# Optimization experiments

Measured on AMD Instinct MI355X. Metric: run time of the kernel, lower is better.

The kernel has to match this reference:

```python
import jax, jax.numpy as jnp
import numpy as np

B, N, P_CTR, K = 16, 2048, 256, 32
H, W = 24, 80
INFEA = 64
MLP = [64, 128, 128, 256]
DIST = 0.5
EPS = 1e-5


def setup_inputs() -> dict:
    key = jax.random.key(0)
    ks = jax.random.split(key, 12)
    inp = {}
    inp['pc'] = jax.random.normal(ks[0], (B, 3, N), jnp.float32)
    inp['feat'] = jax.random.normal(ks[1], (B, INFEA, N), jnp.float32)
    inp['img1'] = jax.random.normal(ks[2], (B, MLP[0], H, W), jnp.float32)
    inp['img2'] = jax.random.normal(ks[3], (B, MLP[1], H, W), jnp.float32)
    inp['P'] = jax.random.normal(ks[4], (B, 3, 4), jnp.float32)
    inp['query_v1'] = jax.random.randint(ks[5], (B, N), 0, H * W, dtype=jnp.int32)
    inp['new_pc'] = jax.random.normal(ks[6], (B, 3, P_CTR), jnp.float32)
    dims = [INFEA + 3] + MLP  # conv chain: 67->64->128->128->256, 1x1 convs, no bias
    for i in range(4):
        fan_in = dims[i]
        inp[f'w{i+1}'] = jax.random.normal(ks[7 + i], (dims[i + 1], dims[i]), jnp.float32) * np.sqrt(2.0 / fan_in)
        inp[f'g{i+1}'] = jnp.ones((dims[i + 1],), jnp.float32)   # BN gamma, init 1
        inp[f'b{i+1}'] = jnp.zeros((dims[i + 1],), jnp.float32)  # BN beta, init 0
    return inp


def query_depth_point(pc, new_pc, dist, k):
    # depth (z-axis) ball query: pc (B,3,N), new_pc (B,3,P) -> idx (B,P,k) int32, num (B,P)
    dz = jnp.abs(pc[:, 2, None, :] - new_pc[:, 2, :, None])  # (B,P,N)
    mask = dz < dist
    num = jnp.sum(mask, axis=-1).astype(jnp.int32)           # neighbor count per center
    # stable argsort of ~mask puts valid indices first, in ascending original order
    order = jnp.argsort(jnp.logical_not(mask), axis=-1, stable=True)
    idx = order[..., :k]
    slot_valid = jnp.arange(k)[None, None, :] < jnp.minimum(num, k)[..., None]
    idx = jnp.where(slot_valid, idx, idx[..., :1])           # pad with first valid index
    return idx.astype(jnp.int32), num


def gather_ch(x, idx):
    # x (B,C,M), idx (B,L) -> (B,C,L)
    return jnp.take_along_axis(x, idx[:, None, :], axis=2)


def conv_bn_relu(x, w, g, b):
    # 1x1 conv (no bias) + BatchNorm2d (training-mode batch stats) + ReLU
    y = jnp.einsum('oc,bcnk->bonk', w, x)
    m = jnp.mean(y, axis=(0, 2, 3), keepdims=True)
    v = jnp.var(y, axis=(0, 2, 3), keepdims=True)
    y = (y - m) * jax.lax.rsqrt(v + EPS)
    y = y * g[None, :, None, None] + b[None, :, None, None]
    return jax.nn.relu(y)


def reference(pc, feat, img1, img2, P, query_v1, new_pc,
              w1, g1, b1, w2, g2, b2, w3, g3, b3, w4, g4, b4):
    idx, num = query_depth_point(pc, new_pc, DIST, K)       # (B,P,K), (B,P)
    idx_flat = idx.reshape(B, P_CTR * K)
    idx_rgb = jnp.take_along_axis(query_v1, idx_flat, axis=1)  # (B,P*K) pixel ids

    grouped_pc = gather_ch(pc, idx_flat).reshape(B, 3, P_CTR, K) - new_pc[:, :, :, None]
    grouped_feat = gather_ch(feat, idx_flat).reshape(B, INFEA, P_CTR, K)
    rgb1 = gather_ch(img1.reshape(B, MLP[0], H * W), idx_rgb).reshape(B, MLP[0], P_CTR, K)
    rgb2 = gather_ch(img2.reshape(B, MLP[1], H * W), idx_rgb).reshape(B, MLP[1], P_CTR, K)

    grouped = jnp.concatenate([grouped_pc, grouped_feat], axis=1)  # (B,67,P,K)
    pf = conv_bn_relu(grouped, w1, g1, b1)                         # (B,64,P,K)
    f1 = jnp.concatenate([pf, rgb1], axis=1)                       # (B,128,P,K)
    pf = conv_bn_relu(pf, w2, g2, b2)                              # (B,128,P,K)
    f2 = jnp.concatenate([pf, rgb2], axis=1)                       # (B,256,P,K)
    pf = conv_bn_relu(pf, w3, g3, b3)
    pf = conv_bn_relu(pf, w4, g4, b4)                              # (B,256,P,K)
    out = jnp.concatenate([f1, f2, pf], axis=1)                    # (B,640,P,K)
    valid = (num > 0).reshape(B, 1, P_CTR, 1).astype(out.dtype)
    return out * valid
```

## Files before the change

### kernel.cpp

```cpp
#include <hip/hip_runtime.h>
#include <hip/hip_fp16.h>

#define BB 16
#define NN 2048
#define PC 256
#define KK 32
#define HWS 1920
#define PT (BB*PC*KK)
#define EPSF 1e-5f
#define THR 512

#define CH_IDXR 256
#define CH_IDX  257
#define CH_VAL  258
#define CH_FT   356
#define STATS_OFF ((size_t)259 << 13)

typedef _Float16 f16x8 __attribute__((ext_vector_type(8)));
typedef float    f32x4 __attribute__((ext_vector_type(4)));

__device__ __forceinline__ unsigned packh2(float lo, float hi) {
  unsigned a = (unsigned)__half_as_ushort(__float2half(lo));
  unsigned b = (unsigned)__half_as_ushort(__float2half(hi));
  return a | (b << 16);
}
__device__ __forceinline__ float h2lo(unsigned u) {
  return __half2float(__ushort_as_half((unsigned short)(u & 0xffffu)));
}
__device__ __forceinline__ float h2hi(unsigned u) {
  return __half2float(__ushort_as_half((unsigned short)(u >> 16)));
}
__device__ __forceinline__ void nt_store4(float* p, float4 v) {
  __builtin_nontemporal_store(v.x, p);
  __builtin_nontemporal_store(v.y, p+1);
  __builtin_nontemporal_store(v.z, p+2);
  __builtin_nontemporal_store(v.w, p+3);
}
__device__ __forceinline__ void nt_store1(float* p, float v) {
  __builtin_nontemporal_store(v, p);
}

__global__ __launch_bounds__(256,2) void k_prep(
    const float* __restrict__ feat, float* out)
{
  __shared__ float tile[64][261];
  int tid = threadIdx.x;
  int b = blockIdx.x >> 3, n0 = (blockIdx.x & 7) << 8;
  #pragma unroll 8
  for (int c = 0; c < 64; c++)
    tile[c][tid] = feat[((size_t)b*64 + c)*NN + n0 + tid];
  __syncthreads();
  unsigned* ftw = (unsigned*)out + (((size_t)b*640 + CH_FT)<<13);
  #pragma unroll
  for (int e = tid; e < 256*32; e += 256) {
    int q = e & 31, nl = e >> 5;
    ftw[(size_t)(n0 + nl)*32 + q] = packh2(tile[2*q][nl], tile[2*q+1][nl]);
  }
}

template<bool WSC>
__global__ __launch_bounds__(256) void k_idx(
    const float* __restrict__ pc, const float* __restrict__ npc,
    const int* __restrict__ qv1, float* out, int* __restrict__ wsi)
{
  __shared__ int slots[4][KK];
  int tid = threadIdx.x;
  if (blockIdx.x < 5) {
    int i = blockIdx.x*256 + tid;
    if (i < 1152) out[STATS_OFF + i] = 0.0f;
  }
  int wl = tid >> 6, lane = tid & 63;
  int w = blockIdx.x*4 + wl;
  int b = w >> 8, p = w & 255;
  if (lane == 0) slots[wl][0] = 0;
  float zc = npc[(b*3+2)*PC + p];
  const float* pz = pc + ((size_t)b*3+2)*NN;
  int num = 0;
  for (int ci=0; ci<NN/64; ci++) {
    int n = ci*64 + lane;
    bool m = fabsf(pz[n] - zc) < 0.5f;
    unsigned long long mk = __ballot(m);
    if (m) {
      int rank = num + __popcll(mk & ((1ull<<lane)-1ull));
      if (rank < KK) slots[wl][rank] = n;
    }
    num += __popcll(mk);
  }
  __syncthreads();
  if (lane < KK) {
    int nj = (lane < num) ? slots[wl][lane] : slots[wl][0];
    size_t col = (size_t)p*KK + lane;
    int enc = (num > 0) ? qv1[b*NN + nj] : -1;
    ((int*)out)[(((size_t)b*640 + CH_IDX )<<13) + col] = nj;
    ((int*)out)[(((size_t)b*640 + CH_IDXR)<<13) + col] = enc;
    if constexpr (WSC) wsi[(size_t)b*8192 + col] = enc;
  }
  if (lane == 0)
    out[(((size_t)b*640 + CH_VAL)<<13) + (size_t)p*KK] = (num > 0) ? 1.0f : 0.0f;
}

template<int CIN, int CINP, int COUT, int BOCH, int WVP, int WVO, int WFP, int WFO,
         int XMODE, int XBASE, int YMODE, int YBASE, int STIN, int STOUT,
         int SWZ, int QR, int PFB, int TILES>
__global__ __launch_bounds__(THR,4) void k_mfma(
    const float* __restrict__ pc, const float* __restrict__ npc,
    const float* __restrict__ W,
    const float* __restrict__ g, const float* __restrict__ bv,
    const float* __restrict__ go, const float* __restrict__ bo,
    float* out)
{
  constexpr int KC = CINP/32;
  constexpr int KCIN = (XMODE == 1) ? CIN/32 : 1;
  __shared__ __align__(16) _Float16 xs[2][128*QR*2];
  __shared__ float scs[128], shs[128];
  __shared__ float redu[WVP*BOCH*2];
  __shared__ float ost[(YMODE==3) ? 2*BOCH : 1];

  int tid = threadIdx.x;
  int tile0 = blockIdx.x * TILES;
  int b = tile0 >> 6;
  int och0 = blockIdx.y * BOCH;

  int wv = tid >> 6, lane = tid & 63;
  int wp = wv % WVP, wo = wv / WVP;
  int lr = lane & 15, lg = lane >> 4;
  int prow0 = wp*(WFP*16), orow0 = wo*(WFO*16);

  unsigned rg[(XMODE==0)?8:1];
  float    pa = 0.f, pb = 0.f, na = 0.f, nb = 0.f;
  uint4    rgv[KCIN];

  auto LOADR = [&](int t) {
    int col0t = ((tile0 + t) & 63) << 7;
    if constexpr (XMODE == 0) {
      int posl = tid & 127, qb0 = tid >> 7;
      int n = ((const int*)out)[(((size_t)b*640 + CH_IDX)<<13) + col0t + posl];
      const unsigned* ftw = (const unsigned*)out + (((size_t)b*640 + CH_FT)<<13);
      #pragma unroll
      for (int k = 0; k < 8; k++)
        rg[k] = ftw[(size_t)n*32 + qb0 + 4*k];
      int pcol = (col0t + posl) >> 5;
      pa = pb = na = nb = 0.f;
      if (qb0 == 0) {
        pa = pc[((size_t)b*3+0)*NN + n]; na = npc[(b*3+0)*PC + pcol];
        pb = pc[((size_t)b*3+1)*NN + n]; nb = npc[(b*3+1)*PC + pcol];
      } else if (qb0 == 1) {
        pa = pc[((size_t)b*3+2)*NN + n]; na = npc[(b*3+2)*PC + pcol];
      }
    } else {
      #pragma unroll
      for (int k = 0; k < KCIN; k++) {
        int e = tid + k*THR;
        int q = e >> 5, pg = e & 31;
        rgv[k] = *(const uint4*)&((const unsigned*)out)[(((size_t)b*640 + XBASE + q)<<13) + col0t + pg*4];
      }
    }
  };

  auto STORE = [&](int t) {
    int col0t = ((tile0 + t) & 63) << 7;
    unsigned* xw = (unsigned*)xs[t & 1];
    if constexpr (XMODE == 0) {
      int posl = tid & 127, qb0 = tid >> 7;
      #pragma unroll
      for (int k = 0; k < 8; k++) {
        int q = qb0 + 4*k;
        int qs = (((q>>2) ^ ((posl>>2) & SWZ)) << 2) | (q & 3);
        xw[posl*QR + qs] = rg[k];
      }
      #pragma unroll
      for (int k = 8; k < 12; k++) {
        int q = qb0 + 4*k;
        unsigned u = 0u;
        if (k == 8) {
          if (qb0 == 0)      u = packh2(pa - na, pb - nb);
          else if (qb0 == 1) u = packh2(pa - na, 0.f);
        }
        int qs = (((q>>2) ^ ((posl>>2) & SWZ)) << 2) | (q & 3);
        xw[posl*QR + qs] = u;
      }
    } else {
      #pragma unroll
      for (int k = 0; k < KCIN; k++) {
        int e = tid + k*THR;
        int q = e >> 5, pg = e & 31;
        uint4 u = rgv[k];
        float s0 = scs[2*q], h0 = shs[2*q], s1 = scs[2*q+1], h1 = shs[2*q+1];
        unsigned uu[4] = {u.x, u.y, u.z, u.w};
        float lo_a[4], hi_a[4];
        #pragma unroll
        for (int j = 0; j < 4; j++) {
          lo_a[j] = fmaxf(fmaf(h2lo(uu[j]), s0, h0), 0.f);
          hi_a[j] = fmaxf(fmaf(h2hi(uu[j]), s1, h1), 0.f);
          int p = pg*4 + j;
          xw[p*QR + ((((q>>2) ^ ((p>>2) & SWZ)) << 2) | (q & 3))] = packh2(lo_a[j], hi_a[j]);
        }
        if constexpr (PFB >= 0) {
          float vv = out[(((size_t)b*640 + CH_VAL)<<13) + col0t + ((pg >> 3) << 5)];
          float4 L  = {lo_a[0]*vv, lo_a[1]*vv, lo_a[2]*vv, lo_a[3]*vv};
          float4 Hh = {hi_a[0]*vv, hi_a[1]*vv, hi_a[2]*vv, hi_a[3]*vv};
          size_t pb2 = (((size_t)b*640 + PFB + 2*q)<<13) + col0t + pg*4;
          nt_store4(&out[pb2],           L);
          nt_store4(&out[pb2 + (1<<13)], Hh);
        }
      }
    }
  };

  LOADR(0);

  f16x8 bfr[KC][WFO];
  #pragma unroll
  for (int kc = 0; kc < KC; kc++)
    #pragma unroll
    for (int fo = 0; fo < WFO; fo++) {
      int orow = och0 + orow0 + fo*16 + lr;
      f16x8 tf;
      if constexpr (XMODE == 0) {
        #pragma unroll
        for (int j = 0; j < 8; j++) {
          int c = kc*32 + lg*8 + j;
          int r = (c < 64) ? c + 3 : (c < 67 ? c - 64 : -1);
          tf[j] = (_Float16)((r >= 0) ? W[(size_t)orow*CIN + r] : 0.f);
        }
      } else {
        const float* wr = W + (size_t)orow*CIN + kc*32 + lg*8;
        float4 w0 = *(const float4*)wr;
        float4 w1 = *(const float4*)(wr + 4);
        tf[0]=(_Float16)w0.x; tf[1]=(_Float16)w0.y; tf[2]=(_Float16)w0.z; tf[3]=(_Float16)w0.w;
        tf[4]=(_Float16)w1.x; tf[5]=(_Float16)w1.y; tf[6]=(_Float16)w1.z; tf[7]=(_Float16)w1.w;
      }
      bfr[kc][fo] = tf;
    }

  if constexpr (XMODE == 1) {
    const float* stin = out + STATS_OFF + STIN;
    for (int c = tid; c < CIN; c += THR) {
      float m   = stin[c] * (1.0f/PT);
      float var = stin[CIN+c]*(1.0f/PT) - m*m;
      float s = rsqrtf(var + EPSF) * g[c];
      scs[c] = s; shs[c] = bv[c] - m*s;
    }
  }
  if constexpr (YMODE == 3) {
    const float* sto = out + STATS_OFF + STOUT;
    for (int i = tid; i < 2*BOCH; i += THR) {
      int gi = (i < BOCH) ? (och0 + i) : (COUT + och0 + (i - BOCH));
      ost[i] = sto[gi];
    }
  }
  __syncthreads();
  float osc_[WFO], osh_[WFO];
  if constexpr (YMODE == 3) {
    #pragma unroll
    for (int fo = 0; fo < WFO; fo++) {
      int oloc = orow0 + fo*16 + lr;
      float m   = ost[oloc]*(1.0f/PT);
      float var = ost[BOCH+oloc]*(1.0f/PT) - m*m;
      float s = rsqrtf(var + EPSF) * go[och0 + oloc];
      osc_[fo] = s; osh_[fo] = bo[och0 + oloc] - m*s;
    }
  }

  STORE(0);
  __syncthreads();

  float ssum[WFO], ssq[WFO];
  #pragma unroll
  for (int fo = 0; fo < WFO; fo++) { ssum[fo] = 0.f; ssq[fo] = 0.f; }

  #pragma unroll
  for (int t = 0; t < TILES; t++) {
    int col0t = ((tile0 + t) & 63) << 7;
    const _Float16* xb = xs[t & 1];

    if (t + 1 < TILES) LOADR(t + 1);

    f32x4 acc[WFP][WFO];
    const f32x4 zero4 = {0.f, 0.f, 0.f, 0.f};
    #pragma unroll
    for (int fp = 0; fp < WFP; fp++)
      #pragma unroll
      for (int fo = 0; fo < WFO; fo++) acc[fp][fo] = zero4;

    #pragma unroll
    for (int kc = 0; kc < KC; kc++) {
      f16x8 af[WFP];
      #pragma unroll
      for (int fp = 0; fp < WFP; fp++) {
        int row = prow0 + fp*16 + lr;
        int qb = (kc*4 + lg) ^ ((row>>2) & SWZ);
        af[fp] = *(const f16x8*)&xb[row*(QR*2) + qb*8];
      }
      #pragma unroll
      for (int fp = 0; fp < WFP; fp++)
        #pragma unroll
        for (int fo = 0; fo < WFO; fo++)
          acc[fp][fo] = __builtin_amdgcn_mfma_f32_16x16x32_f16(af[fp], bfr[kc][fo], acc[fp][fo], 0, 0, 0);
    }

    if constexpr (YMODE == 1) {
      #pragma unroll
      for (int fp = 0; fp < WFP; fp++) {
        int pos = col0t + prow0 + fp*16 + lg*4;
        #pragma unroll
        for (int fo = 0; fo < WFO; fo++) {
          float pr0 = __shfl_xor(acc[fp][fo][0], 1);
          float pr1 = __shfl_xor(acc[fp][fo][1], 1);
          float pr2 = __shfl_xor(acc[fp][fo][2], 1);
          float pr3 = __shfl_xor(acc[fp][fo][3], 1);
          if (!(lane & 1)) {
            uint4 u;
            u.x = packh2(acc[fp][fo][0], pr0); u.y = packh2(acc[fp][fo][1], pr1);
            u.z = packh2(acc[fp][fo][2], pr2); u.w = packh2(acc[fp][fo][3], pr3);
            int qrow = (och0 + orow0 + fo*16 + lr) >> 1;
            *(uint4*)&((unsigned*)out)[(((size_t)b*640 + YBASE + qrow)<<13) + pos] = u;
          }
        }
      }
    } else if constexpr (YMODE == 3) {
      #pragma unroll
      for (int fp = 0; fp < WFP; fp++) {
        int pos = col0t + prow0 + fp*16 + lg*4;
        float v = out[(((size_t)b*640 + CH_VAL)<<13) + (pos & ~31)];
        #pragma unroll
        for (int fo = 0; fo < WFO; fo++) {
          int och = och0 + orow0 + fo*16 + lr;
          float4 wvv;
          wvv.x = fmaxf(fmaf(acc[fp][fo][0], osc_[fo], osh_[fo]), 0.f) * v;
          wvv.y = fmaxf(fmaf(acc[fp][fo][1], osc_[fo], osh_[fo]), 0.f) * v;
          wvv.z = fmaxf(fmaf(acc[fp][fo][2], osc_[fo], osh_[fo]), 0.f) * v;
          wvv.w = fmaxf(fmaf(acc[fp][fo][3], osc_[fo], osh_[fo]), 0.f) * v;
          nt_store4(&out[(((size_t)b*640 + YBASE + och)<<13) + pos], wvv);
        }
      }
    }

    if constexpr (YMODE != 3) {
      #pragma unroll
      for (int fo = 0; fo < WFO; fo++)
        #pragma unroll
        for (int fp = 0; fp < WFP; fp++)
          #pragma unroll
          for (int r = 0; r < 4; r++) {
            float v = acc[fp][fo][r];
            ssum[fo] += v; ssq[fo] += v*v;
          }
    }

    if (t + 1 < TILES) STORE(t + 1);
    __syncthreads();
  }

  if constexpr (YMODE != 3) {
    #pragma unroll
    for (int fo = 0; fo < WFO; fo++) {
      float s = ssum[fo], q2 = ssq[fo];
      s  += __shfl_down(s, 32);  s  += __shfl_down(s, 16);
      q2 += __shfl_down(q2, 32); q2 += __shfl_down(q2, 16);
      if (lane < 16) {
        int oloc = orow0 + fo*16 + lane;
        redu[(wp*BOCH + oloc)*2]     = s;
        redu[(wp*BOCH + oloc)*2 + 1] = q2;
      }
    }
    __syncthreads();
    float* stg = out + STATS_OFF + STOUT;
    for (int i = tid; i < BOCH; i += THR) {
      float ss = 0.f, qq = 0.f;
      #pragma unroll
      for (int p = 0; p < WVP; p++) { ss += redu[(p*BOCH + i)*2]; qq += redu[(p*BOCH + i)*2 + 1]; }
      atomicAdd(&stg[och0 + i], ss);
      atomicAdd(&stg[COUT + och0 + i], qq);
    }
  }
}

__global__ __launch_bounds__(512) void k_rgb_lds(
    const float* __restrict__ img1, const float* __restrict__ img2,
    const int* __restrict__ wsi, float* out)
{
  __shared__ float ls[4][HWS];
  int tid = threadIdx.x;
  int b = blockIdx.x / 48, gq = blockIdx.x % 48;
  int gc0 = gq * 4;
  for (int e = tid; e < 4*(HWS/4); e += 512) {
    int c = e / (HWS/4), off = e % (HWS/4);
    int gc = gc0 + c;
    const float* src = (gc < 64) ? img1 + ((size_t)b*64 + gc)*HWS
                                 : img2 + ((size_t)b*128 + (gc-64))*HWS;
    *(float4*)&ls[c][off*4] = *(const float4*)&src[off*4];
  }
  __syncthreads();
  const int* idr = wsi + (size_t)b*8192;
  int dch0 = (gc0 < 64) ? 64 + gc0 : 256 + (gc0 - 64);
  for (int pp = tid; pp < 8192; pp += 512) {
    int enc = idr[pp];
    float v = (enc >= 0) ? 1.0f : 0.0f;
    int ir  = (enc >= 0) ? enc : 0;
    #pragma unroll
    for (int c = 0; c < 4; c++)
      nt_store1(&out[(((size_t)b*640 + dch0 + c)<<13) + pp], ls[c][ir] * v);
  }
}

__global__ __launch_bounds__(256) void k_rgb_fb(
    const float* __restrict__ img1, const float* __restrict__ img2, float* out)
{
  int tid = threadIdx.x;
  int pos = blockIdx.x*256 + tid;
  int b = pos >> 13, rem = pos & 8191;
  int enc = ((const int*)out)[(((size_t)b*640 + CH_IDXR)<<13) + rem];
  float v  = (enc >= 0) ? 1.0f : 0.0f;
  int  ir  = (enc >= 0) ? enc : 0;
  size_t o1 = (((size_t)b*640 + 64)<<13) + rem;
  const float* i1 = img1 + (size_t)b*64*HWS + ir;
  #pragma unroll 8
  for (int c=0;c<64;c++) out[o1 + ((size_t)c<<13)] = i1[(size_t)c*HWS] * v;
  size_t o2 = (((size_t)b*640 + 256)<<13) + rem;
  const float* i2 = img2 + (size_t)b*128*HWS + ir;
  #pragma unroll 8
  for (int c=0;c<128;c++) out[o2 + ((size_t)c<<13)] = i2[(size_t)c*HWS] * v;
}

extern "C" void kernel_launch(void* const* d_in, const int* in_sizes, int n_in,
                              void* d_out, int out_size, void* d_ws, size_t ws_size,
                              hipStream_t stream)
{
  const float* pc   = (const float*)d_in[0];
  const float* feat = (const float*)d_in[1];
  const float* img1 = (const float*)d_in[2];
  const float* img2 = (const float*)d_in[3];
  const int*   qv1  = (const int*)d_in[5];
  const float* npc  = (const float*)d_in[6];
  const float* w1 = (const float*)d_in[7];
  const float* g1 = (const float*)d_in[8];
  const float* b1 = (const float*)d_in[9];
  const float* w2 = (const float*)d_in[10];
  const float* g2 = (const float*)d_in[11];
  const float* b2 = (const float*)d_in[12];
  const float* w3 = (const float*)d_in[13];
  const float* g3 = (const float*)d_in[14];
  const float* b3 = (const float*)d_in[15];
  const float* w4 = (const float*)d_in[16];
  const float* g4 = (const float*)d_in[17];
  const float* b4 = (const float*)d_in[18];
  float* out = (float*)d_out;
  int*  wsi = (int*)d_ws;
  const bool use_ws = (d_ws != nullptr) && (ws_size >= (size_t)BB*8192*4);

  k_prep <<<128,256,0,stream>>>(feat, out);
  if (use_ws) k_idx<true ><<<1024,256,0,stream>>>(pc, npc, qv1, out, wsi);
  else        k_idx<false><<<1024,256,0,stream>>>(pc, npc, qv1, out, wsi);
  k_mfma<67,96,64,64,    2,4,4,1, 0,0,   1,324, 0,0,     0,48, -1,1>
      <<<dim3(1024,1),THR,0,stream>>>(pc,npc,w1,g1,b1,g1,b1,out);
  k_mfma<64,64,128,128,  2,4,4,2, 1,324, 1,260, 0,128,   7,36, 0,1>
      <<<dim3(1024,1),THR,0,stream>>>(pc,npc,w2,g1,b1,g1,b1,out);
  k_mfma<128,128,128,128,2,4,4,2, 1,260, 1,64,  128,384, 7,68, 128,1>
      <<<dim3(1024,1),THR,0,stream>>>(pc,npc,w3,g2,b2,g2,b2,out);
  k_mfma<128,128,256,128,2,4,4,2, 1,64,  2,0,   384,640, 7,68, -1,1>
      <<<dim3(1024,2),THR,0,stream>>>(pc,npc,w4,g3,b3,g3,b3,out);
  k_mfma<128,128,256,128,2,4,4,2, 1,64,  3,384, 384,640, 7,68, -1,1>
      <<<dim3(1024,2),THR,0,stream>>>(pc,npc,w4,g3,b3,g4,b4,out);
  if (use_ws) k_rgb_lds<<<768,512,0,stream>>>(img1, img2, wsi, out);
  else        k_rgb_fb <<<512,256,0,stream>>>(img1, img2, out);
}
```

Measured before the change: 579.1 us.

## Move intermediates to workspace, fuse RGB gather into conv3, two tiles per block

Intermediate fp16 activations, validity flags and BN stats now live in a separate workspace instead of scratch channels inside the output tensor. The RGB image gather is merged into the conv3 launch by interleaving extra gather blocks (3 of every 5) with conv blocks, so it runs alongside the GEMM work and one launch disappears. Every conv kernel now processes two tiles per block at half the grid size. The cost is a larger workspace requirement, a fallback path kept for small workspaces, and more complex block-role dispatch with shared memory overlaid between the two roles.

```diff
diff --git a/kernel.cpp b/kernel.cpp
--- a/kernel.cpp
+++ b/kernel.cpp
@@ -61,16 +61,19 @@
 template<bool WSC>
 __global__ __launch_bounds__(256) void k_idx(
     const float* __restrict__ pc, const float* __restrict__ npc,
-    const int* __restrict__ qv1, float* out, int* __restrict__ wsi)
+    const int* __restrict__ qv1, float* out, int* __restrict__ wsi,
+    float* __restrict__ wsval, float* __restrict__ wsst)
 {
   __shared__ int slots[4][KK];
   int tid = threadIdx.x;
-  if (blockIdx.x < 5) {
-    int i = blockIdx.x*256 + tid;
+  int bx = blockIdx.x;
+  if (bx < 5) {
+    int i = bx*256 + tid;
     if (i < 1152) out[STATS_OFF + i] = 0.0f;
+    if (wsst && i < 1152) wsst[i] = 0.0f;
   }
   int wl = tid >> 6, lane = tid & 63;
-  int w = blockIdx.x*4 + wl;
+  int w = bx*4 + wl;
   int b = w >> 8, p = w & 255;
   if (lane == 0) slots[wl][0] = 0;
   float zc = npc[(b*3+2)*PC + p];
@@ -95,29 +98,79 @@
     ((int*)out)[(((size_t)b*640 + CH_IDXR)<<13) + col] = enc;
     if constexpr (WSC) wsi[(size_t)b*8192 + col] = enc;
   }
-  if (lane == 0)
-    out[(((size_t)b*640 + CH_VAL)<<13) + (size_t)p*KK] = (num > 0) ? 1.0f : 0.0f;
-}
-
-template<int CIN, int CINP, int COUT, int BOCH, int WVP, int WVO, int WFP, int WFO,
-         int XMODE, int XBASE, int YMODE, int YBASE, int STIN, int STOUT,
-         int SWZ, int QR, int PFB, int TILES>
+  if (lane == 0) {
+    float v = (num > 0) ? 1.0f : 0.0f;
+    out[(((size_t)b*640 + CH_VAL)<<13) + (size_t)p*KK] = v;
+    if constexpr (WSC) if (wsval) wsval[(size_t)b*8192 + (size_t)p*KK] = v;
+  }
+}
+
+template<int CIN,int CINP,int COUT,int BOCH,int WVP,int WVO,int WFP,int WFO,
+         int XMODE,int YMODE,int SWZ,int QR,bool HASPF,int TILES,
+         int XROWS,int YROWS,int VROWS,int RGBN>
 __global__ __launch_bounds__(THR,4) void k_mfma(
     const float* __restrict__ pc, const float* __restrict__ npc,
     const float* __restrict__ W,
     const float* __restrict__ g, const float* __restrict__ bv,
     const float* __restrict__ go, const float* __restrict__ bo,
-    float* out)
+    const float* __restrict__ stin_p, float* __restrict__ stout_p,
+    const unsigned* __restrict__ xbuf, unsigned* __restrict__ ybuf,
+    float* __restrict__ yf32, float* __restrict__ pfb,
+    const float* __restrict__ valb,
+    const float* __restrict__ img1, const float* __restrict__ img2,
+    const int* __restrict__ wsi, float* out)
 {
   constexpr int KC = CINP/32;
   constexpr int KCIN = (XMODE == 1) ? CIN/32 : 1;
-  __shared__ __align__(16) _Float16 xs[2][128*QR*2];
-  __shared__ float scs[128], shs[128];
-  __shared__ float redu[WVP*BOCH*2];
-  __shared__ float ost[(YMODE==3) ? 2*BOCH : 1];
+  constexpr size_t XS_B = (size_t)128*QR*8;
+  constexpr size_t SC_B = 1024;
+  constexpr size_t RD_B = (size_t)WVP*BOCH*2*4;
+  constexpr size_t OS_B = (YMODE==3) ? (size_t)2*BOCH*4 : 16;
+  constexpr size_t CONV_B = XS_B + SC_B + RD_B + OS_B;
+  constexpr size_t RGB_B  = (RGBN>0) ? (size_t)4*HWS*4 : 0;
+  constexpr size_t SM_B   = (CONV_B > RGB_B) ? CONV_B : RGB_B;
+  __shared__ __align__(16) char smraw[SM_B];
 
   int tid = threadIdx.x;
-  int tile0 = blockIdx.x * TILES;
+  int bx = blockIdx.x;
+  int cid;
+  if constexpr (RGBN > 0) {
+    int m5 = bx % 5;
+    if (m5 >= 2) {
+      int rid = (bx/5)*3 + (m5-2);
+      float (*ls)[HWS] = (float(*)[HWS])smraw;
+      int b2 = rid / 48, gq = rid % 48;
+      int gc0 = gq*4;
+      for (int e = tid; e < 4*(HWS/4); e += THR) {
+        int c = e/(HWS/4), off = e%(HWS/4);
+        int gc = gc0 + c;
+        const float* src = (gc < 64) ? img1 + ((size_t)b2*64 + gc)*HWS
+                                     : img2 + ((size_t)b2*128 + (gc-64))*HWS;
+        *(float4*)&ls[c][off*4] = *(const float4*)&src[off*4];
+      }
+      __syncthreads();
+      const int* idr = wsi + (size_t)b2*8192;
+      int dch0 = (gc0 < 64) ? 64 + gc0 : 256 + (gc0 - 64);
+      for (int pp = tid; pp < 8192; pp += THR) {
+        int enc = idr[pp];
+        float v = (enc >= 0) ? 1.0f : 0.0f;
+        int ir  = (enc >= 0) ? enc : 0;
+        #pragma unroll
+        for (int c = 0; c < 4; c++)
+          nt_store1(&out[(((size_t)b2*640 + dch0 + c)<<13) + pp], ls[c][ir] * v);
+      }
+      return;
+    }
+    cid = (bx/5)*2 + m5;
+  } else cid = bx;
+
+  _Float16* xsb = (_Float16*)smraw;
+  float* scs  = (float*)(smraw + XS_B);
+  float* shs  = scs + 128;
+  float* redu = (float*)(smraw + XS_B + SC_B);
+  float* ost  = (float*)(smraw + XS_B + SC_B + RD_B);
+
+  int tile0 = cid * TILES;
   int b = tile0 >> 6;
   int och0 = blockIdx.y * BOCH;
 
@@ -152,14 +205,14 @@
       for (int k = 0; k < KCIN; k++) {
         int e = tid + k*THR;
         int q = e >> 5, pg = e & 31;
-        rgv[k] = *(const uint4*)&((const unsigned*)out)[(((size_t)b*640 + XBASE + q)<<13) + col0t + pg*4];
+        rgv[k] = *(const uint4*)&xbuf[(((size_t)b*XROWS + q)<<13) + col0t + pg*4];
       }
     }
   };
 
   auto STORE = [&](int t) {
     int col0t = ((tile0 + t) & 63) << 7;
-    unsigned* xw = (unsigned*)xs[t & 1];
+    unsigned* xw = (unsigned*)(xsb + (t & 1)*(128*QR*2));
     if constexpr (XMODE == 0) {
       int posl = tid & 127, qb0 = tid >> 7;
       #pragma unroll
@@ -195,13 +248,13 @@
           int p = pg*4 + j;
           xw[p*QR + ((((q>>2) ^ ((p>>2) & SWZ)) << 2) | (q & 3))] = packh2(lo_a[j], hi_a[j]);
         }
-        if constexpr (PFB >= 0) {
-          float vv = out[(((size_t)b*640 + CH_VAL)<<13) + col0t + ((pg >> 3) << 5)];
+        if constexpr (HASPF) {
+          float vv = valb[(((size_t)b*VROWS)<<13) + col0t + ((pg >> 3) << 5)];
           float4 L  = {lo_a[0]*vv, lo_a[1]*vv, lo_a[2]*vv, lo_a[3]*vv};
           float4 Hh = {hi_a[0]*vv, hi_a[1]*vv, hi_a[2]*vv, hi_a[3]*vv};
-          size_t pb2 = (((size_t)b*640 + PFB + 2*q)<<13) + col0t + pg*4;
-          nt_store4(&out[pb2],           L);
-          nt_store4(&out[pb2 + (1<<13)], Hh);
+          size_t pb2 = (((size_t)b*640 + 2*q)<<13) + col0t + pg*4;
+          nt_store4(&pfb[pb2],           L);
+          nt_store4(&pfb[pb2 + (1<<13)], Hh);
         }
       }
     }
@@ -234,19 +287,17 @@
     }
 
   if constexpr (XMODE == 1) {
-    const float* stin = out + STATS_OFF + STIN;
     for (int c = tid; c < CIN; c += THR) {
-      float m   = stin[c] * (1.0f/PT);
-      float var = stin[CIN+c]*(1.0f/PT) - m*m;
+      float m   = stin_p[c] * (1.0f/PT);
+      float var = stin_p[CIN+c]*(1.0f/PT) - m*m;
       float s = rsqrtf(var + EPSF) * g[c];
       scs[c] = s; shs[c] = bv[c] - m*s;
     }
   }
   if constexpr (YMODE == 3) {
-    const float* sto = out + STATS_OFF + STOUT;
     for (int i = tid; i < 2*BOCH; i += THR) {
       int gi = (i < BOCH) ? (och0 + i) : (COUT + och0 + (i - BOCH));
-      ost[i] = sto[gi];
+      ost[i] = stout_p[gi];
     }
   }
   __syncthreads();
@@ -272,7 +323,7 @@
   #pragma unroll
   for (int t = 0; t < TILES; t++) {
     int col0t = ((tile0 + t) & 63) << 7;
-    const _Float16* xb = xs[t & 1];
+    const _Float16* xb = xsb + (t & 1)*(128*QR*2);
 
     if (t + 1 < TILES) LOADR(t + 1);
 
@@ -314,7 +365,7 @@
             u.x = packh2(acc[fp][fo][0], pr0); u.y = packh2(acc[fp][fo][1], pr1);
             u.z = packh2(acc[fp][fo][2], pr2); u.w = packh2(acc[fp][fo][3], pr3);
             int qrow = (och0 + orow0 + fo*16 + lr) >> 1;
-            *(uint4*)&((unsigned*)out)[(((size_t)b*640 + YBASE + qrow)<<13) + pos] = u;
+            *(uint4*)&ybuf[(((size_t)b*YROWS + qrow)<<13) + pos] = u;
           }
         }
       }
@@ -322,7 +373,7 @@
       #pragma unroll
       for (int fp = 0; fp < WFP; fp++) {
         int pos = col0t + prow0 + fp*16 + lg*4;
-        float v = out[(((size_t)b*640 + CH_VAL)<<13) + (pos & ~31)];
+        float v = valb[(((size_t)b*VROWS)<<13) + (pos & ~31)];
         #pragma unroll
         for (int fo = 0; fo < WFO; fo++) {
           int och = och0 + orow0 + fo*16 + lr;
@@ -331,7 +382,7 @@
           wvv.y = fmaxf(fmaf(acc[fp][fo][1], osc_[fo], osh_[fo]), 0.f) * v;
           wvv.z = fmaxf(fmaf(acc[fp][fo][2], osc_[fo], osh_[fo]), 0.f) * v;
           wvv.w = fmaxf(fmaf(acc[fp][fo][3], osc_[fo], osh_[fo]), 0.f) * v;
-          nt_store4(&out[(((size_t)b*640 + YBASE + och)<<13) + pos], wvv);
+          nt_store4(&yf32[(((size_t)b*640 + och)<<13) + pos], wvv);
         }
       }
     }
@@ -365,13 +416,12 @@
       }
     }
     __syncthreads();
-    float* stg = out + STATS_OFF + STOUT;
     for (int i = tid; i < BOCH; i += THR) {
       float ss = 0.f, qq = 0.f;
       #pragma unroll
       for (int p = 0; p < WVP; p++) { ss += redu[(p*BOCH + i)*2]; qq += redu[(p*BOCH + i)*2 + 1]; }
-      atomicAdd(&stg[och0 + i], ss);
-      atomicAdd(&stg[COUT + och0 + i], qq);
+      atomicAdd(&stout_p[och0 + i], ss);
+      atomicAdd(&stout_p[COUT + och0 + i], qq);
     }
   }
 }
@@ -427,6 +477,7 @@
                               void* d_out, int out_size, void* d_ws, size_t ws_size,
                               hipStream_t stream)
 {
+  (void)in_sizes; (void)n_in;
   const float* pc   = (const float*)d_in[0];
   const float* feat = (const float*)d_in[1];
   const float* img1 = (const float*)d_in[2];
@@ -446,22 +497,71 @@
   const float* g4 = (const float*)d_in[17];
   const float* b4 = (const float*)d_in[18];
   float* out = (float*)d_out;
-  int*  wsi = (int*)d_ws;
-  const bool use_ws = (d_ws != nullptr) && (ws_size >= (size_t)BB*8192*4);
+  unsigned* outu = (unsigned*)d_out;
+
+  const size_t W_IDXR = (size_t)BB*8192;
+  const size_t W_Y    = (size_t)BB*64*8192;
+  const size_t NEED_SMALL = W_IDXR*4;
+  const size_t NEED_BIG   = (W_IDXR*2 + 1152)*4 + 2*W_Y*4;
+  int*      wsi  = (int*)d_ws;
+  float*    wsval= (float*)d_ws + W_IDXR;
+  float*    wsst = wsval + W_IDXR;
+  unsigned* wsy2 = (unsigned*)((float*)d_ws + 2*W_IDXR + 1152);
+  unsigned* wsy3 = wsy2 + W_Y;
+  const bool small_ws = (d_ws != nullptr) && (ws_size >= NEED_SMALL);
+  const bool big_ws   = (d_ws != nullptr) && (ws_size >= NEED_BIG);
+
+  float* ost_ = out + STATS_OFF;
 
   k_prep <<<128,256,0,stream>>>(feat, out);
-  if (use_ws) k_idx<true ><<<1024,256,0,stream>>>(pc, npc, qv1, out, wsi);
-  else        k_idx<false><<<1024,256,0,stream>>>(pc, npc, qv1, out, wsi);
-  k_mfma<67,96,64,64,    2,4,4,1, 0,0,   1,324, 0,0,     0,48, -1,1>
-      <<<dim3(1024,1),THR,0,stream>>>(pc,npc,w1,g1,b1,g1,b1,out);
-  k_mfma<64,64,128,128,  2,4,4,2, 1,324, 1,260, 0,128,   7,36, 0,1>
-      <<<dim3(1024,1),THR,0,stream>>>(pc,npc,w2,g1,b1,g1,b1,out);
-  k_mfma<128,128,128,128,2,4,4,2, 1,260, 1,64,  128,384, 7,68, 128,1>
-      <<<dim3(1024,1),THR,0,stream>>>(pc,npc,w3,g2,b2,g2,b2,out);
-  k_mfma<128,128,256,128,2,4,4,2, 1,64,  2,0,   384,640, 7,68, -1,1>
-      <<<dim3(1024,2),THR,0,stream>>>(pc,npc,w4,g3,b3,g3,b3,out);
-  k_mfma<128,128,256,128,2,4,4,2, 1,64,  3,384, 384,640, 7,68, -1,1>
-      <<<dim3(1024,2),THR,0,stream>>>(pc,npc,w4,g3,b3,g4,b4,out);
-  if (use_ws) k_rgb_lds<<<768,512,0,stream>>>(img1, img2, wsi, out);
-  else        k_rgb_fb <<<512,256,0,stream>>>(img1, img2, out);
-}
+  if (small_ws) k_idx<true ><<<1024,256,0,stream>>>(pc,npc,qv1,out,wsi, big_ws?wsval:nullptr, big_ws?wsst:nullptr);
+  else          k_idx<false><<<1024,256,0,stream>>>(pc,npc,qv1,out,nullptr,nullptr,nullptr);
+
+  if (big_ws) {
+    k_mfma<67,96,64,64, 2,4,4,1, 0,1, 0,48, false,2, 640,640,1,0>
+      <<<dim3(512,1),THR,0,stream>>>(pc,npc,w1,g1,b1,g1,b1,
+        wsst, wsst+0, outu, outu + ((size_t)324<<13), nullptr, nullptr,
+        wsval, nullptr,nullptr,nullptr, out);
+    k_mfma<64,64,128,128, 2,4,4,2, 1,1, 7,36, true,2, 640,64,1,0>
+      <<<dim3(512,1),THR,0,stream>>>(pc,npc,w2,g1,b1,g1,b1,
+        wsst+0, wsst+128, outu + ((size_t)324<<13), wsy2, nullptr, out,
+        wsval, nullptr,nullptr,nullptr, out);
+    k_mfma<128,128,128,128, 2,4,4,2, 1,1, 7,68, true,2, 64,64,1,768>
+      <<<dim3(1280,1),THR,0,stream>>>(pc,npc,w3,g2,b2,g2,b2,
+        wsst+128, wsst+384, wsy2, wsy3, nullptr, out + ((size_t)128<<13),
+        wsval, img1,img2,wsi, out);
+    k_mfma<128,128,256,128, 2,4,4,2, 1,2, 7,68, false,2, 64,640,1,0>
+      <<<dim3(512,2),THR,0,stream>>>(pc,npc,w4,g3,b3,g3,b3,
+        wsst+384, wsst+640, wsy3, nullptr, nullptr, nullptr,
+        wsval, nullptr,nullptr,nullptr, out);
+    k_mfma<128,128,256,128, 2,4,4,2, 1,3, 7,68, false,2, 64,640,1,0>
+      <<<dim3(512,2),THR,0,stream>>>(pc,npc,w4,g3,b3,g4,b4,
+        wsst+384, wsst+640, wsy3, nullptr, out + ((size_t)384<<13), nullptr,
+        wsval, nullptr,nullptr,nullptr, out);
+  } else {
+    k_mfma<67,96,64,64, 2,4,4,1, 0,1, 0,48, false,2, 640,640,640,0>
+      <<<dim3(512,1),THR,0,stream>>>(pc,npc,w1,g1,b1,g1,b1,
+        ost_, ost_+0, outu, outu + ((size_t)324<<13), nullptr, nullptr,
+        out + ((size_t)258<<13), nullptr,nullptr,nullptr, out);
+    k_mfma<64,64,128,128, 2,4,4,2, 1,1, 7,36, true,2, 640,640,640,0>
+      <<<dim3(512,1),THR,0,stream>>>(pc,npc,w2,g1,b1,g1,b1,
+        ost_+0, ost_+128, outu + ((size_t)324<<13), outu + ((size_t)260<<13),
+        nullptr, out, out + ((size_t)258<<13), nullptr,nullptr,nullptr, out);
+    k_mfma<128,128,128,128, 2,4,4,2, 1,1, 7,68, true,2, 640,640,640,0>
+      <<<dim3(512,1),THR,0,stream>>>(pc,npc,w3,g2,b2,g2,b2,
+        ost_+128, ost_+384, outu + ((size_t)260<<13), outu + ((size_t)64<<13),
+        nullptr, out + ((size_t)128<<13), out + ((size_t)258<<13),
+        nullptr,nullptr,nullptr, out);
+    k_mfma<128,128,256,128, 2,4,4,2, 1,2, 7,68, false,2, 640,640,640,0>
+      <<<dim3(512,2),THR,0,stream>>>(pc,npc,w4,g3,b3,g3,b3,
+        ost_+384, ost_+640, outu + ((size_t)64<<13), nullptr, nullptr, nullptr,
+        out + ((size_t)258<<13), nullptr,nullptr,nullptr, out);
+    k_mfma<128,128,256,128, 2,4,4,2, 1,3, 7,68, false,2, 640,640,640,0>
+      <<<dim3(512,2),THR,0,stream>>>(pc,npc,w4,g3,b3,g4,b4,
+        ost_+384, ost_+640, outu + ((size_t)64<<13), nullptr,
+        out + ((size_t)384<<13), nullptr, out + ((size_t)258<<13),
+        nullptr,nullptr,nullptr, out);
+    if (small_ws) k_rgb_lds<<<768,512,0,stream>>>(img1, img2, wsi, out);
+    else          k_rgb_fb <<<512,256,0,stream>>>(img1, img2, out);
+  }
+}
```

After: 551.4 us. -4.8%, faster.
